# Performance work log

Hardware: AMD Instinct MI355X
Metric: run time of the kernel (lower is better)

## Reference

```python
import jax, jax.numpy as jnp
import numpy as np

B, Q, F, D, H = 16384, 1024, 2, 5, 4  # batch, n_qubits, n_features, depth, heads


def setup_inputs() -> dict:
    key = jax.random.key(0)
    ks = iter(jax.random.split(key, 16))
    def rnd(shape, s=0.02):
        return jax.random.normal(next(ks), shape, dtype=jnp.float32) * s
    return {
        "x": jax.random.normal(next(ks), (B, F), dtype=jnp.float32),
        # amplitude_encoder: Linear(F,4Q) -> LN -> GELU -> Linear(4Q,2Q) -> LN -> Tanh -> Linear(2Q,Q)
        "amp_W1": rnd((4 * Q, F)), "amp_b1": jnp.zeros((4 * Q,), jnp.float32),
        "amp_g1": jnp.ones((4 * Q,), jnp.float32), "amp_be1": jnp.zeros((4 * Q,), jnp.float32),
        "amp_W2": rnd((2 * Q, 4 * Q)), "amp_b2": jnp.zeros((2 * Q,), jnp.float32),
        "amp_g2": jnp.ones((2 * Q,), jnp.float32), "amp_be2": jnp.zeros((2 * Q,), jnp.float32),
        "amp_W3": rnd((Q, 2 * Q)), "amp_b3": jnp.zeros((Q,), jnp.float32),
        # phase_encoder: Linear(F,2Q) -> LN -> SiLU -> Linear(2Q,Q) -> Tanh
        "ph_W1": rnd((2 * Q, F)), "ph_b1": jnp.zeros((2 * Q,), jnp.float32),
        "ph_g1": jnp.ones((2 * Q,), jnp.float32), "ph_be1": jnp.zeros((2 * Q,), jnp.float32),
        "ph_W2": rnd((Q, 2 * Q)), "ph_b2": jnp.zeros((Q,), jnp.float32),
        # rotation parameters (depth, Q, 3); only the last depth slice survives the overwrite loop
        "rot_freq": jax.random.normal(next(ks), (D, Q, 3), dtype=jnp.float32),
        "rot_phase": jax.random.normal(next(ks), (D, Q, 3), dtype=jnp.float32),
        # MultiheadAttention(Q, 4 heads)
        "attn_in_w": rnd((3 * Q, Q)), "attn_in_b": jnp.zeros((3 * Q,), jnp.float32),
        "attn_out_w": rnd((Q, Q)), "attn_out_b": jnp.zeros((Q,), jnp.float32),
    }


def _ln(x, g, b):
    m = jnp.mean(x, -1, keepdims=True)
    v = jnp.mean((x - m) ** 2, -1, keepdims=True)
    return (x - m) * jax.lax.rsqrt(v + 1e-5) * g + b


def reference(x, amp_W1, amp_b1, amp_g1, amp_be1, amp_W2, amp_b2, amp_g2, amp_be2,
              amp_W3, amp_b3, ph_W1, ph_b1, ph_g1, ph_be1, ph_W2, ph_b2,
              rot_freq, rot_phase, attn_in_w, attn_in_b, attn_out_w, attn_out_b):
    # amplitude encoder (Dropout is identity in eval mode)
    h = jax.nn.gelu(_ln(x @ amp_W1.T + amp_b1, amp_g1, amp_be1), approximate=False)
    h = jnp.tanh(_ln(h @ amp_W2.T + amp_b2, amp_g2, amp_be2))
    amp = h @ amp_W3.T + amp_b3                      # (B, Q)
    # phase encoder
    p = jax.nn.silu(_ln(x @ ph_W1.T + ph_b1, ph_g1, ph_be1))
    phase = jnp.tanh(p @ ph_W2.T + ph_b2)            # (B, Q)
    # multiscale conv branch: n_features=2 < min kernel size 3 => skipped, combined_conv = 0
    # depth loop overwrites quantum_state each iteration => only depth index D-1 matters
    rx = jnp.sin(amp * rot_freq[-1, :, 0] + rot_phase[-1, :, 0])
    ry = jnp.cos(phase * rot_freq[-1, :, 1] + rot_phase[-1, :, 1])
    rz = jnp.broadcast_to(jnp.tanh(rot_phase[-1, :, 2]), rx.shape)  # tanh(0*f + p)
    qs = (rx + ry + rz) / 3.0                        # (B, Q)
    # MultiheadAttention with seq_len == 1: softmax over a single key is exactly 1,
    # so attended output == V projection regardless of Q/K.
    qkv = qs @ attn_in_w.T + attn_in_b               # (B, 3Q)
    v = qkv[:, 2 * Q:]                               # (B, Q)
    return v @ attn_out_w.T + attn_out_b
```

## Files before the change

kernel.cpp:

```cpp
#include <hip/hip_runtime.h>

using bf16x8 = __attribute__((ext_vector_type(8))) __bf16;
using u16x8  = __attribute__((ext_vector_type(8))) unsigned short;
using f32x4  = __attribute__((ext_vector_type(4))) float;

__device__ __forceinline__ unsigned short f2bf(float f){
  unsigned int u = __float_as_uint(f);
  u += 0x7fffu + ((u >> 16) & 1u);
  return (unsigned short)(u >> 16);
}
__device__ __forceinline__ float bf2f(unsigned short h){
  return __uint_as_float(((unsigned int)h) << 16);
}

__global__ __launch_bounds__(256) void cvt_bf16(const float* __restrict__ s,
                                                unsigned short* __restrict__ d, int n){
  int i = blockIdx.x * 256 + threadIdx.x;
  if (i < n) d[i] = f2bf(s[i]);
}

__global__ __launch_bounds__(256) void front_amp_kernel(
    const float* __restrict__ x,
    const float* __restrict__ W1, const float* __restrict__ b1,
    const float* __restrict__ g1, const float* __restrict__ be1,
    unsigned short* __restrict__ h)
{
  __shared__ float red[256];
  __shared__ float red2[256];
  __shared__ float s_mean, s_inv;
  const int row = blockIdx.x;
  const int tid = threadIdx.x;
  const float x0 = x[row * 2 + 0];
  const float x1 = x[row * 2 + 1];

  const f32x4* W4 = (const f32x4*)(W1 + (size_t)tid * 32);
  float va[16];
  float sum = 0.f, sq = 0.f;
#pragma unroll
  for (int i4 = 0; i4 < 4; i4++){
    f32x4 b4 = *(const f32x4*)(b1 + tid * 16 + i4 * 4);
    f32x4 wa = W4[i4 * 2], wb = W4[i4 * 2 + 1];
    float v0 = x0 * wa[0] + x1 * wa[1] + b4[0];
    float v1 = x0 * wa[2] + x1 * wa[3] + b4[1];
    float v2 = x0 * wb[0] + x1 * wb[1] + b4[2];
    float v3 = x0 * wb[2] + x1 * wb[3] + b4[3];
    va[i4*4+0] = v0; va[i4*4+1] = v1; va[i4*4+2] = v2; va[i4*4+3] = v3;
    sum += v0 + v1 + v2 + v3;
    sq  += v0*v0 + v1*v1 + v2*v2 + v3*v3;
  }
  red[tid] = sum; red2[tid] = sq; __syncthreads();
  for (int s = 128; s > 0; s >>= 1){
    if (tid < s){ red[tid] += red[tid + s]; red2[tid] += red2[tid + s]; }
    __syncthreads();
  }
  if (tid == 0){
    float m = red[0] * (1.0f / 4096.0f);
    float v = red2[0] * (1.0f / 4096.0f) - m * m;
    s_mean = m; s_inv = rsqrtf(v + 1e-5f);
  }
  __syncthreads();
  float mean = s_mean, inv = s_inv;
#pragma unroll
  for (int i8 = 0; i8 < 2; i8++){
    f32x4 ga = *(const f32x4*)(g1  + tid * 16 + i8 * 8);
    f32x4 gb = *(const f32x4*)(g1  + tid * 16 + i8 * 8 + 4);
    f32x4 ba = *(const f32x4*)(be1 + tid * 16 + i8 * 8);
    f32x4 bb = *(const f32x4*)(be1 + tid * 16 + i8 * 8 + 4);
    u16x8 o;
#pragma unroll
    for (int k = 0; k < 8; k++){
      float gk = (k < 4) ? ga[k] : gb[k - 4];
      float bk = (k < 4) ? ba[k] : bb[k - 4];
      float y = (va[i8 * 8 + k] - mean) * inv * gk + bk;
      float ge = 0.5f * y * (1.0f + erff(y * 0.70710678118654752f));
      o[k] = f2bf(ge);
    }
    *(u16x8*)&h[(size_t)row * 4096 + tid * 16 + i8 * 8] = o;
  }
}

__global__ __launch_bounds__(256) void front_ph_kernel(
    const float* __restrict__ x,
    const float* __restrict__ W1, const float* __restrict__ b1,
    const float* __restrict__ g1, const float* __restrict__ be1,
    unsigned short* __restrict__ p)
{
  __shared__ float red[256];
  __shared__ float red2[256];
  __shared__ float s_mean, s_inv;
  const int row = blockIdx.x;
  const int tid = threadIdx.x;
  const float x0 = x[row * 2 + 0];
  const float x1 = x[row * 2 + 1];

  const f32x4* W4 = (const f32x4*)(W1 + (size_t)tid * 16);
  float vp[8];
  float sum = 0.f, sq = 0.f;
#pragma unroll
  for (int i4 = 0; i4 < 2; i4++){
    f32x4 b4 = *(const f32x4*)(b1 + tid * 8 + i4 * 4);
    f32x4 wa = W4[i4 * 2], wb = W4[i4 * 2 + 1];
    float v0 = x0 * wa[0] + x1 * wa[1] + b4[0];
    float v1 = x0 * wa[2] + x1 * wa[3] + b4[1];
    float v2 = x0 * wb[0] + x1 * wb[1] + b4[2];
    float v3 = x0 * wb[2] + x1 * wb[3] + b4[3];
    vp[i4*4+0] = v0; vp[i4*4+1] = v1; vp[i4*4+2] = v2; vp[i4*4+3] = v3;
    sum += v0 + v1 + v2 + v3;
    sq  += v0*v0 + v1*v1 + v2*v2 + v3*v3;
  }
  red[tid] = sum; red2[tid] = sq; __syncthreads();
  for (int s = 128; s > 0; s >>= 1){
    if (tid < s){ red[tid] += red[tid + s]; red2[tid] += red2[tid + s]; }
    __syncthreads();
  }
  if (tid == 0){
    float m = red[0] * (1.0f / 2048.0f);
    float v = red2[0] * (1.0f / 2048.0f) - m * m;
    s_mean = m; s_inv = rsqrtf(v + 1e-5f);
  }
  __syncthreads();
  float mean = s_mean, inv = s_inv;
  {
    f32x4 ga = *(const f32x4*)(g1  + tid * 8);
    f32x4 gb = *(const f32x4*)(g1  + tid * 8 + 4);
    f32x4 ba = *(const f32x4*)(be1 + tid * 8);
    f32x4 bb = *(const f32x4*)(be1 + tid * 8 + 4);
    u16x8 o;
#pragma unroll
    for (int k = 0; k < 8; k++){
      float gk = (k < 4) ? ga[k] : gb[k - 4];
      float bk = (k < 4) ? ba[k] : bb[k - 4];
      float y = (vp[k] - mean) * inv * gk + bk;
      float si = y / (1.0f + expf(-y));
      o[k] = f2bf(si);
    }
    *(u16x8*)&p[(size_t)row * 2048 + tid * 8] = o;
  }
}

__global__ __launch_bounds__(256) void ln_tanh_kernel(
    unsigned short* __restrict__ c, const float* __restrict__ g,
    const float* __restrict__ be)
{
  __shared__ float red[256];
  __shared__ float red2[256];
  __shared__ float s_mean, s_inv;
  const size_t base = (size_t)blockIdx.x * 2048;
  const int tid = threadIdx.x;
  u16x8 cv = *(const u16x8*)&c[base + tid * 8];
  float v[8];
  float sum = 0.f, sq = 0.f;
#pragma unroll
  for (int k = 0; k < 8; k++){
    float t = bf2f(cv[k]);
    v[k] = t; sum += t; sq += t * t;
  }
  red[tid] = sum; red2[tid] = sq; __syncthreads();
  for (int s = 128; s > 0; s >>= 1){
    if (tid < s){ red[tid] += red[tid + s]; red2[tid] += red2[tid + s]; }
    __syncthreads();
  }
  if (tid == 0){
    float m = red[0] * (1.0f / 2048.0f);
    float vv = red2[0] * (1.0f / 2048.0f) - m * m;
    s_mean = m; s_inv = rsqrtf(vv + 1e-5f);
  }
  __syncthreads();
  float mean = s_mean, inv = s_inv;
  {
    f32x4 ga = *(const f32x4*)(g  + tid * 8);
    f32x4 gb = *(const f32x4*)(g  + tid * 8 + 4);
    f32x4 ba = *(const f32x4*)(be + tid * 8);
    f32x4 bb = *(const f32x4*)(be + tid * 8 + 4);
    u16x8 o;
#pragma unroll
    for (int k = 0; k < 8; k++){
      float gk = (k < 4) ? ga[k] : gb[k - 4];
      float bk = (k < 4) ? ba[k] : bb[k - 4];
      float y = (v[k] - mean) * inv * gk + bk;
      o[k] = f2bf(tanhf(y));
    }
    *(u16x8*)&c[base + tid * 8] = o;
  }
}


#define WAITV4() asm volatile("s_waitcnt vmcnt(4)" ::: "memory")
#define WAITV8() asm volatile("s_waitcnt vmcnt(8)" ::: "memory")
#define WAITV0() asm volatile("s_waitcnt vmcnt(0)" ::: "memory")

template<int EPI>
__global__ __launch_bounds__(512, 2) void gemm_bt(
    const unsigned short* __restrict__ A, const unsigned short* __restrict__ B,
    void* __restrict__ outp, int M, int N, int K, int nT,
    const float* __restrict__ bias,
    const float* __restrict__ aux0, const float* __restrict__ aux1,
    const unsigned short* __restrict__ aux2)
{
  __shared__ __align__(16) char smem_raw[131072];
  unsigned short* S = (unsigned short*)smem_raw;

  const int tid  = threadIdx.x;
  const int wave = tid >> 6, lane = tid & 63;
  const int wm = wave >> 1, wn = wave & 1;
  const int lm = lane & 15, lq = lane >> 4;

  int lid = blockIdx.x;
  {
    const int nwg = gridDim.x;
    if ((nwg & 7) == 0) lid = (lid & 7) * (nwg >> 3) + (lid >> 3);
  }
  const int m0 = (lid / nT) * 256, n0 = (lid % nT) * 256;

  f32x4 acc[4][8];
#pragma unroll
  for (int i = 0; i < 4; i++)
#pragma unroll
    for (int j = 0; j < 8; j++) acc[i][j] = (f32x4){0.f, 0.f, 0.f, 0.f};

  const int lr = lane >> 2;
  const int lc = (((lane & 3) ^ ((lr >> 1) & 3)) << 3);
  const unsigned short* gA = A + (size_t)(m0 + wave * 32 + lr) * K + lc;
  const unsigned short* gB = B + (size_t)(n0 + wave * 32 + lr) * K + lc;
  const size_t rowK16 = (size_t)16 * K;

  auto stage = [&](int buf){
    unsigned short* lA = S + buf * 16384 + wave * 1024;
    unsigned short* lB = lA + 8192;
    __builtin_amdgcn_global_load_lds(
        (const __attribute__((address_space(1))) void*)gA,
        (__attribute__((address_space(3))) void*)lA, 16, 0, 0);
    __builtin_amdgcn_global_load_lds(
        (const __attribute__((address_space(1))) void*)(gA + rowK16),
        (__attribute__((address_space(3))) void*)(lA + 512), 16, 0, 0);
    __builtin_amdgcn_global_load_lds(
        (const __attribute__((address_space(1))) void*)gB,
        (__attribute__((address_space(3))) void*)lB, 16, 0, 0);
    __builtin_amdgcn_global_load_lds(
        (const __attribute__((address_space(1))) void*)(gB + rowK16),
        (__attribute__((address_space(3))) void*)(lB + 512), 16, 0, 0);
    gA += 32; gB += 32;
  };

  auto readA = [&](int buf, bf16x8* af){
    const unsigned short* sA = S + buf * 16384;
#pragma unroll
    for (int q = 0; q < 4; q++){
      const int r = wm * 64 + q * 16 + lm;
      af[q] = *(const bf16x8*)&sA[r * 32 + ((lq ^ ((r >> 1) & 3)) << 3)];
    }
  };
  auto readB = [&](int buf, bf16x8* bfr){
    const unsigned short* sB = S + buf * 16384 + 8192;
#pragma unroll
    for (int q = 0; q < 8; q++){
      const int r = wn * 128 + q * 16 + lm;
      bfr[q] = *(const bf16x8*)&sB[r * 32 + ((lq ^ ((r >> 1) & 3)) << 3)];
    }
  };

  auto mfmaAll = [&](const bf16x8* af, const bf16x8* bfr){
    __builtin_amdgcn_s_setprio(1);
#pragma unroll
    for (int i = 0; i < 4; i++)
#pragma unroll
      for (int j = 0; j < 8; j++)
        acc[i][j] = __builtin_amdgcn_mfma_f32_16x16x32_bf16(af[i], bfr[j], acc[i][j], 0, 0, 0);
    __builtin_amdgcn_s_setprio(0);
  };

  const int nTk = K >> 5;
  bf16x8 af[4], bfA[8], bfB[8];
  stage(0); stage(1); stage(2);
  WAITV8();
  __builtin_amdgcn_s_barrier();
  readB(0, bfA);
  for (int t = 0; t < nTk; t += 2){
    if (t + 2 < nTk) WAITV4(); else WAITV0();
    __builtin_amdgcn_s_barrier();
    if (t + 3 < nTk) stage((t + 3) & 3);
    readA(t & 3, af);
    readB((t + 1) & 3, bfB);
    __builtin_amdgcn_sched_barrier(0);
    mfmaAll(af, bfA);
    if (t + 2 < nTk){
      if (t + 3 < nTk) WAITV4(); else WAITV0();
    }
    __builtin_amdgcn_s_barrier();
    if (t + 4 < nTk) stage((t + 4) & 3);
    readA((t + 1) & 3, af);
    if (t + 2 < nTk) readB((t + 2) & 3, bfA);
    __builtin_amdgcn_sched_barrier(0);
    mfmaAll(af, bfB);
  }

  __syncthreads();
  float* ew = (float*)smem_raw + wave * 2112;

#pragma unroll
  for (int i = 0; i < 4; i++){
#pragma unroll
    for (int j = 0; j < 8; j++){
      const int col = n0 + wn * 128 + j * 16 + lm;
      float bcol = bias[col];
      float f0 = 0.f, p0 = 0.f, rzv = 0.f;
      if constexpr (EPI == 1){
        f0 = aux0[3 * col]; p0 = aux1[3 * col]; rzv = tanhf(aux1[3 * col + 2]);
      }
      if constexpr (EPI == 2){
        f0 = aux0[3 * col + 1]; p0 = aux1[3 * col + 1];
      }
#pragma unroll
      for (int r = 0; r < 4; r++){
        const float val = acc[i][j][r];
        float pre;
        if constexpr (EPI == 0 || EPI == 3)      pre = val + bcol;
        else if constexpr (EPI == 1)             pre = sinf((val + bcol) * f0 + p0) + rzv;
        else                                     pre = cosf(tanhf(val + bcol) * f0 + p0);
        ew[(lq * 4 + r) * 132 + j * 16 + lm] = pre;
      }
    }
    if constexpr (EPI != 3){
#pragma unroll
      for (int s = 0; s < 4; s++){
        const int lrow = 4 * s + lq;
        const int grow = m0 + wm * 64 + i * 16 + lrow;
        const float* src = ew + lrow * 132 + lm * 8;
        f32x4 v0 = *(const f32x4*)(src);
        f32x4 v1 = *(const f32x4*)(src + 4);
        const size_t gidx = (size_t)grow * N + n0 + wn * 128 + lm * 8;
        u16x8 o;
        if constexpr (EPI == 1){
          u16x8 ry8 = *(const u16x8*)&aux2[gidx];
#pragma unroll
          for (int t = 0; t < 4; t++){
            o[t]     = f2bf((v0[t] + bf2f(ry8[t]))     * (1.0f / 3.0f));
            o[t + 4] = f2bf((v1[t] + bf2f(ry8[t + 4])) * (1.0f / 3.0f));
          }
        } else {
#pragma unroll
          for (int t = 0; t < 4; t++){
            o[t] = f2bf(v0[t]); o[t + 4] = f2bf(v1[t]);
          }
        }
        *(u16x8*)&((unsigned short*)outp)[gidx] = o;
      }
    } else {
#pragma unroll
      for (int s = 0; s < 8; s++){
        const int lrow = 2 * s + (lane >> 5);
        const int grow = m0 + wm * 64 + i * 16 + lrow;
        const int lcol = (lane & 31) * 4;
        f32x4 v = *(const f32x4*)(ew + lrow * 132 + lcol);
        *(f32x4*)&((float*)outp)[(size_t)grow * N + n0 + wn * 128 + lcol] = v;
      }
    }
  }
}

extern "C" void kernel_launch(void* const* d_in, const int* in_sizes, int n_in,
                              void* d_out, int out_size, void* d_ws, size_t ws_size,
                              hipStream_t stream)
{
  const float* x    = (const float*)d_in[0];
  const float* aW1  = (const float*)d_in[1];
  const float* ab1  = (const float*)d_in[2];
  const float* ag1  = (const float*)d_in[3];
  const float* abe1 = (const float*)d_in[4];
  const float* aW2  = (const float*)d_in[5];
  const float* ab2  = (const float*)d_in[6];
  const float* ag2  = (const float*)d_in[7];
  const float* abe2 = (const float*)d_in[8];
  const float* aW3  = (const float*)d_in[9];
  const float* ab3  = (const float*)d_in[10];
  const float* pW1  = (const float*)d_in[11];
  const float* pb1  = (const float*)d_in[12];
  const float* pg1  = (const float*)d_in[13];
  const float* pbe1 = (const float*)d_in[14];
  const float* pW2  = (const float*)d_in[15];
  const float* pb2  = (const float*)d_in[16];
  const float* rfreq  = (const float*)d_in[17];
  const float* rphase = (const float*)d_in[18];
  const float* aiw  = (const float*)d_in[19];
  const float* aib  = (const float*)d_in[20];
  const float* aow  = (const float*)d_in[21];
  const float* aob  = (const float*)d_in[22];

  const int B = 16384, Q = 1024;

  char* ws = (char*)d_ws;
  size_t off = 0;
  auto alloc = [&](size_t bytes) -> char* {
    char* ptr = ws + off; off += (bytes + 255) & ~(size_t)255; return ptr;
  };
  unsigned short* Wb2  = (unsigned short*)alloc((size_t)2 * Q * 4 * Q * 2);
  unsigned short* Wb3  = (unsigned short*)alloc((size_t)Q * 2 * Q * 2);
  unsigned short* PWb2 = (unsigned short*)alloc((size_t)Q * 2 * Q * 2);
  unsigned short* WVb  = (unsigned short*)alloc((size_t)Q * Q * 2);
  unsigned short* WOb  = (unsigned short*)alloc((size_t)Q * Q * 2);
  unsigned short* R1   = (unsigned short*)alloc((size_t)B * 4 * Q * 2);
  unsigned short* ry   = (unsigned short*)alloc((size_t)B * Q * 2);

  unsigned short* p  = R1;
  unsigned short* h  = R1;
  unsigned short* qs = R1;
  unsigned short* v  = R1 + (size_t)B * Q;
  unsigned short* c2 = (unsigned short*)d_out;

  cvt_bf16<<<(2*Q*4*Q + 255) / 256, 256, 0, stream>>>(aW2, Wb2, 2*Q*4*Q);
  cvt_bf16<<<(Q*2*Q + 255) / 256, 256, 0, stream>>>(aW3, Wb3, Q*2*Q);
  cvt_bf16<<<(Q*2*Q + 255) / 256, 256, 0, stream>>>(pW2, PWb2, Q*2*Q);
  cvt_bf16<<<(Q*Q + 255) / 256, 256, 0, stream>>>(aiw + (size_t)2*Q*Q, WVb, Q*Q);
  cvt_bf16<<<(Q*Q + 255) / 256, 256, 0, stream>>>(aow, WOb, Q*Q);

  const float* rf4 = rfreq  + (size_t)4 * Q * 3;
  const float* rp4 = rphase + (size_t)4 * Q * 3;

  const int mT = B / 256;
  const int nT1 = 2 * Q / 256;
  const int nTq = Q / 256;

  front_ph_kernel<<<B, 256, 0, stream>>>(x, pW1, pb1, pg1, pbe1, p);
  gemm_bt<2><<<nTq * mT, 512, 0, stream>>>(p, PWb2, ry, B, Q, 2*Q, nTq,
                                           pb2, rf4, rp4, nullptr);

  front_amp_kernel<<<B, 256, 0, stream>>>(x, aW1, ab1, ag1, abe1, h);
  gemm_bt<0><<<nT1 * mT, 512, 0, stream>>>(h, Wb2, c2, B, 2*Q, 4*Q, nT1,
                                           ab2, nullptr, nullptr, nullptr);
  ln_tanh_kernel<<<B, 256, 0, stream>>>(c2, ag2, abe2);

  gemm_bt<1><<<nTq * mT, 512, 0, stream>>>(c2, Wb3, qs, B, Q, 2*Q, nTq,
                                           ab3, rf4, rp4, ry);
  gemm_bt<0><<<nTq * mT, 512, 0, stream>>>(qs, WVb, v, B, Q, Q, nTq,
                                           aib + 2*Q, nullptr, nullptr, nullptr);
  gemm_bt<3><<<nTq * mT, 512, 0, stream>>>(v, WOb, d_out, B, Q, Q, nTq,
                                           aob, nullptr, nullptr, nullptr);
}
```

Before: 928.8 us.

## Precompute first-layer LayerNorm moments from weight statistics; use wave shuffles in LN

The first Linear has only two input features, so each row's mean and second moment are closed-form functions of x and nine weight/bias moments. A single-block kernel computes those moments once per call, and the front kernels then drop their shared-memory block reductions and barriers. The second LayerNorm (ln_tanh) switches from a tree reduction in shared memory to wave-level xor shuffles plus a small cross-wave sum. The risk is reduced numerical accuracy, because the variance comes from E[x²]−m² built from weight moments.

```diff
diff --git a/kernel.cpp b/kernel.cpp
--- a/kernel.cpp
+++ b/kernel.cpp
@@ -19,61 +19,70 @@
   if (i < n) d[i] = f2bf(s[i]);
 }
 
+__global__ __launch_bounds__(256) void ln_stats_kernel(
+    const float* __restrict__ W, const float* __restrict__ b, int n,
+    float* __restrict__ out)
+{
+  __shared__ float red[9][256];
+  const int tid = threadIdx.x;
+  float a[9] = {0.f,0.f,0.f,0.f,0.f,0.f,0.f,0.f,0.f};
+  for (int j = tid; j < n; j += 256){
+    float w0 = W[2*j], w1 = W[2*j+1], bb = b[j];
+    a[0] += w0;      a[1] += w1;      a[2] += bb;
+    a[3] += w0*w0;   a[4] += w1*w1;   a[5] += bb*bb;
+    a[6] += w0*w1;   a[7] += w0*bb;   a[8] += w1*bb;
+  }
+#pragma unroll
+  for (int k = 0; k < 9; k++) red[k][tid] = a[k];
+  __syncthreads();
+  for (int s = 128; s > 0; s >>= 1){
+    if (tid < s){
+#pragma unroll
+      for (int k = 0; k < 9; k++) red[k][tid] += red[k][tid + s];
+    }
+    __syncthreads();
+  }
+  if (tid < 9) out[tid] = red[tid][0] / (float)n;
+}
+
 __global__ __launch_bounds__(256) void front_amp_kernel(
     const float* __restrict__ x,
     const float* __restrict__ W1, const float* __restrict__ b1,
     const float* __restrict__ g1, const float* __restrict__ be1,
+    const float* __restrict__ st,
     unsigned short* __restrict__ h)
 {
-  __shared__ float red[256];
-  __shared__ float red2[256];
-  __shared__ float s_mean, s_inv;
   const int row = blockIdx.x;
   const int tid = threadIdx.x;
   const float x0 = x[row * 2 + 0];
   const float x1 = x[row * 2 + 1];
+  const float m   = x0 * st[0] + x1 * st[1] + st[2];
+  const float e2  = x0*x0*st[3] + x1*x1*st[4] + st[5]
+                  + 2.0f*(x0*x1*st[6] + x0*st[7] + x1*st[8]);
+  const float inv = rsqrtf(e2 - m * m + 1e-5f);
 
   const f32x4* W4 = (const f32x4*)(W1 + (size_t)tid * 32);
-  float va[16];
-  float sum = 0.f, sq = 0.f;
-#pragma unroll
-  for (int i4 = 0; i4 < 4; i4++){
-    f32x4 b4 = *(const f32x4*)(b1 + tid * 16 + i4 * 4);
-    f32x4 wa = W4[i4 * 2], wb = W4[i4 * 2 + 1];
-    float v0 = x0 * wa[0] + x1 * wa[1] + b4[0];
-    float v1 = x0 * wa[2] + x1 * wa[3] + b4[1];
-    float v2 = x0 * wb[0] + x1 * wb[1] + b4[2];
-    float v3 = x0 * wb[2] + x1 * wb[3] + b4[3];
-    va[i4*4+0] = v0; va[i4*4+1] = v1; va[i4*4+2] = v2; va[i4*4+3] = v3;
-    sum += v0 + v1 + v2 + v3;
-    sq  += v0*v0 + v1*v1 + v2*v2 + v3*v3;
-  }
-  red[tid] = sum; red2[tid] = sq; __syncthreads();
-  for (int s = 128; s > 0; s >>= 1){
-    if (tid < s){ red[tid] += red[tid + s]; red2[tid] += red2[tid + s]; }
-    __syncthreads();
-  }
-  if (tid == 0){
-    float m = red[0] * (1.0f / 4096.0f);
-    float v = red2[0] * (1.0f / 4096.0f) - m * m;
-    s_mean = m; s_inv = rsqrtf(v + 1e-5f);
-  }
-  __syncthreads();
-  float mean = s_mean, inv = s_inv;
 #pragma unroll
   for (int i8 = 0; i8 < 2; i8++){
-    f32x4 ga = *(const f32x4*)(g1  + tid * 16 + i8 * 8);
-    f32x4 gb = *(const f32x4*)(g1  + tid * 16 + i8 * 8 + 4);
-    f32x4 ba = *(const f32x4*)(be1 + tid * 16 + i8 * 8);
-    f32x4 bb = *(const f32x4*)(be1 + tid * 16 + i8 * 8 + 4);
     u16x8 o;
 #pragma unroll
-    for (int k = 0; k < 8; k++){
-      float gk = (k < 4) ? ga[k] : gb[k - 4];
-      float bk = (k < 4) ? ba[k] : bb[k - 4];
-      float y = (va[i8 * 8 + k] - mean) * inv * gk + bk;
-      float ge = 0.5f * y * (1.0f + erff(y * 0.70710678118654752f));
-      o[k] = f2bf(ge);
+    for (int q = 0; q < 2; q++){
+      f32x4 wa = W4[i8 * 4 + q * 2];
+      f32x4 wb = W4[i8 * 4 + q * 2 + 1];
+      f32x4 b4 = *(const f32x4*)(b1  + tid * 16 + i8 * 8 + q * 4);
+      f32x4 g4 = *(const f32x4*)(g1  + tid * 16 + i8 * 8 + q * 4);
+      f32x4 e4 = *(const f32x4*)(be1 + tid * 16 + i8 * 8 + q * 4);
+      float vv[4];
+      vv[0] = x0 * wa[0] + x1 * wa[1] + b4[0];
+      vv[1] = x0 * wa[2] + x1 * wa[3] + b4[1];
+      vv[2] = x0 * wb[0] + x1 * wb[1] + b4[2];
+      vv[3] = x0 * wb[2] + x1 * wb[3] + b4[3];
+#pragma unroll
+      for (int t = 0; t < 4; t++){
+        float y = (vv[t] - m) * inv * g4[t] + e4[t];
+        float ge = 0.5f * y * (1.0f + erff(y * 0.70710678118654752f));
+        o[q * 4 + t] = f2bf(ge);
+      }
     }
     *(u16x8*)&h[(size_t)row * 4096 + tid * 16 + i8 * 8] = o;
   }
@@ -83,68 +92,47 @@
     const float* __restrict__ x,
     const float* __restrict__ W1, const float* __restrict__ b1,
     const float* __restrict__ g1, const float* __restrict__ be1,
+    const float* __restrict__ st,
     unsigned short* __restrict__ p)
 {
-  __shared__ float red[256];
-  __shared__ float red2[256];
-  __shared__ float s_mean, s_inv;
   const int row = blockIdx.x;
   const int tid = threadIdx.x;
   const float x0 = x[row * 2 + 0];
   const float x1 = x[row * 2 + 1];
+  const float m   = x0 * st[0] + x1 * st[1] + st[2];
+  const float e2  = x0*x0*st[3] + x1*x1*st[4] + st[5]
+                  + 2.0f*(x0*x1*st[6] + x0*st[7] + x1*st[8]);
+  const float inv = rsqrtf(e2 - m * m + 1e-5f);
 
   const f32x4* W4 = (const f32x4*)(W1 + (size_t)tid * 16);
-  float vp[8];
-  float sum = 0.f, sq = 0.f;
-#pragma unroll
-  for (int i4 = 0; i4 < 2; i4++){
-    f32x4 b4 = *(const f32x4*)(b1 + tid * 8 + i4 * 4);
-    f32x4 wa = W4[i4 * 2], wb = W4[i4 * 2 + 1];
-    float v0 = x0 * wa[0] + x1 * wa[1] + b4[0];
-    float v1 = x0 * wa[2] + x1 * wa[3] + b4[1];
-    float v2 = x0 * wb[0] + x1 * wb[1] + b4[2];
-    float v3 = x0 * wb[2] + x1 * wb[3] + b4[3];
-    vp[i4*4+0] = v0; vp[i4*4+1] = v1; vp[i4*4+2] = v2; vp[i4*4+3] = v3;
-    sum += v0 + v1 + v2 + v3;
-    sq  += v0*v0 + v1*v1 + v2*v2 + v3*v3;
-  }
-  red[tid] = sum; red2[tid] = sq; __syncthreads();
-  for (int s = 128; s > 0; s >>= 1){
-    if (tid < s){ red[tid] += red[tid + s]; red2[tid] += red2[tid + s]; }
-    __syncthreads();
-  }
-  if (tid == 0){
-    float m = red[0] * (1.0f / 2048.0f);
-    float v = red2[0] * (1.0f / 2048.0f) - m * m;
-    s_mean = m; s_inv = rsqrtf(v + 1e-5f);
-  }
-  __syncthreads();
-  float mean = s_mean, inv = s_inv;
-  {
-    f32x4 ga = *(const f32x4*)(g1  + tid * 8);
-    f32x4 gb = *(const f32x4*)(g1  + tid * 8 + 4);
-    f32x4 ba = *(const f32x4*)(be1 + tid * 8);
-    f32x4 bb = *(const f32x4*)(be1 + tid * 8 + 4);
-    u16x8 o;
-#pragma unroll
-    for (int k = 0; k < 8; k++){
-      float gk = (k < 4) ? ga[k] : gb[k - 4];
-      float bk = (k < 4) ? ba[k] : bb[k - 4];
-      float y = (vp[k] - mean) * inv * gk + bk;
+  u16x8 o;
+#pragma unroll
+  for (int q = 0; q < 2; q++){
+    f32x4 wa = W4[q * 2];
+    f32x4 wb = W4[q * 2 + 1];
+    f32x4 b4 = *(const f32x4*)(b1  + tid * 8 + q * 4);
+    f32x4 g4 = *(const f32x4*)(g1  + tid * 8 + q * 4);
+    f32x4 e4 = *(const f32x4*)(be1 + tid * 8 + q * 4);
+    float vv[4];
+    vv[0] = x0 * wa[0] + x1 * wa[1] + b4[0];
+    vv[1] = x0 * wa[2] + x1 * wa[3] + b4[1];
+    vv[2] = x0 * wb[0] + x1 * wb[1] + b4[2];
+    vv[3] = x0 * wb[2] + x1 * wb[3] + b4[3];
+#pragma unroll
+    for (int t = 0; t < 4; t++){
+      float y = (vv[t] - m) * inv * g4[t] + e4[t];
       float si = y / (1.0f + expf(-y));
-      o[k] = f2bf(si);
-    }
-    *(u16x8*)&p[(size_t)row * 2048 + tid * 8] = o;
-  }
+      o[q * 4 + t] = f2bf(si);
+    }
+  }
+  *(u16x8*)&p[(size_t)row * 2048 + tid * 8] = o;
 }
 
 __global__ __launch_bounds__(256) void ln_tanh_kernel(
     unsigned short* __restrict__ c, const float* __restrict__ g,
     const float* __restrict__ be)
 {
-  __shared__ float red[256];
-  __shared__ float red2[256];
-  __shared__ float s_mean, s_inv;
+  __shared__ float partial[8];
   const size_t base = (size_t)blockIdx.x * 2048;
   const int tid = threadIdx.x;
   u16x8 cv = *(const u16x8*)&c[base + tid * 8];
@@ -155,18 +143,18 @@
     float t = bf2f(cv[k]);
     v[k] = t; sum += t; sq += t * t;
   }
-  red[tid] = sum; red2[tid] = sq; __syncthreads();
-  for (int s = 128; s > 0; s >>= 1){
-    if (tid < s){ red[tid] += red[tid + s]; red2[tid] += red2[tid + s]; }
-    __syncthreads();
-  }
-  if (tid == 0){
-    float m = red[0] * (1.0f / 2048.0f);
-    float vv = red2[0] * (1.0f / 2048.0f) - m * m;
-    s_mean = m; s_inv = rsqrtf(vv + 1e-5f);
-  }
+#pragma unroll
+  for (int off = 32; off > 0; off >>= 1){
+    sum += __shfl_xor(sum, off);
+    sq  += __shfl_xor(sq,  off);
+  }
+  const int wv = tid >> 6;
+  if ((tid & 63) == 0){ partial[wv * 2] = sum; partial[wv * 2 + 1] = sq; }
   __syncthreads();
-  float mean = s_mean, inv = s_inv;
+  const float ts = partial[0] + partial[2] + partial[4] + partial[6];
+  const float tq = partial[1] + partial[3] + partial[5] + partial[7];
+  const float mean = ts * (1.0f / 2048.0f);
+  const float inv  = rsqrtf(tq * (1.0f / 2048.0f) - mean * mean + 1e-5f);
   {
     f32x4 ga = *(const f32x4*)(g  + tid * 8);
     f32x4 gb = *(const f32x4*)(g  + tid * 8 + 4);
@@ -398,6 +386,8 @@
   unsigned short* PWb2 = (unsigned short*)alloc((size_t)Q * 2 * Q * 2);
   unsigned short* WVb  = (unsigned short*)alloc((size_t)Q * Q * 2);
   unsigned short* WOb  = (unsigned short*)alloc((size_t)Q * Q * 2);
+  float* stA = (float*)alloc(64);
+  float* stP = (float*)alloc(64);
   unsigned short* R1   = (unsigned short*)alloc((size_t)B * 4 * Q * 2);
   unsigned short* ry   = (unsigned short*)alloc((size_t)B * Q * 2);
 
@@ -413,6 +403,9 @@
   cvt_bf16<<<(Q*Q + 255) / 256, 256, 0, stream>>>(aiw + (size_t)2*Q*Q, WVb, Q*Q);
   cvt_bf16<<<(Q*Q + 255) / 256, 256, 0, stream>>>(aow, WOb, Q*Q);
 
+  ln_stats_kernel<<<1, 256, 0, stream>>>(pW1, pb1, 2*Q, stP);
+  ln_stats_kernel<<<1, 256, 0, stream>>>(aW1, ab1, 4*Q, stA);
+
   const float* rf4 = rfreq  + (size_t)4 * Q * 3;
   const float* rp4 = rphase + (size_t)4 * Q * 3;
 
@@ -420,11 +413,11 @@
   const int nT1 = 2 * Q / 256;
   const int nTq = Q / 256;
 
-  front_ph_kernel<<<B, 256, 0, stream>>>(x, pW1, pb1, pg1, pbe1, p);
+  front_ph_kernel<<<B, 256, 0, stream>>>(x, pW1, pb1, pg1, pbe1, stP, p);
   gemm_bt<2><<<nTq * mT, 512, 0, stream>>>(p, PWb2, ry, B, Q, 2*Q, nTq,
                                            pb2, rf4, rp4, nullptr);
 
-  front_amp_kernel<<<B, 256, 0, stream>>>(x, aW1, ab1, ag1, abe1, h);
+  front_amp_kernel<<<B, 256, 0, stream>>>(x, aW1, ab1, ag1, abe1, stA, h);
   gemm_bt<0><<<nT1 * mT, 512, 0, stream>>>(h, Wb2, c2, B, 2*Q, 4*Q, nT1,
                                            ab2, nullptr, nullptr, nullptr);
   ln_tanh_kernel<<<B, 256, 0, stream>>>(c2, ag2, abe2);
```

Measured after the change: 971.2 us. 1.05x slower.
